# Kernel optimization log

Measured on AMD Instinct MI355X. Metric: run time of the kernel, lower is better.

The kernel has to match this reference:

```python
import jax, jax.numpy as jnp
import numpy as np
import math

D_MODEL = 1024
NUM_HEADS = 16
HEAD_DIM = D_MODEL // NUM_HEADS  # 64
THETA = 10000.0
BATCH = 2
SEQ = 2048


def setup_inputs() -> dict:
    key = jax.random.key(0)
    ks = jax.random.split(key, 5)
    scale = 0.02
    return {
        "in_features": jax.random.normal(ks[0], (BATCH, SEQ, D_MODEL), jnp.float32),
        "q_proj": jax.random.normal(ks[1], (D_MODEL, D_MODEL), jnp.float32) * scale,
        "k_proj": jax.random.normal(ks[2], (D_MODEL, D_MODEL), jnp.float32) * scale,
        "v_proj": jax.random.normal(ks[3], (D_MODEL, D_MODEL), jnp.float32) * scale,
        "o_proj": jax.random.normal(ks[4], (D_MODEL, D_MODEL), jnp.float32) * scale,
        "token_positions": jnp.arange(SEQ, dtype=jnp.int32),
    }


def _rope(x, token_positions):
    # x: [b, h, s, head_dim]; interleaved even/odd rotation
    half = HEAD_DIM // 2
    inv_freq = 1.0 / (THETA ** (2.0 * jnp.arange(half, dtype=x.dtype) / HEAD_DIM))
    angle = token_positions.astype(x.dtype)[:, None] * inv_freq[None, :]  # [s, half]
    cos, sin = jnp.cos(angle), jnp.sin(angle)
    x_e, x_o = x[..., ::2], x[..., 1::2]
    r_e = x_e * cos - x_o * sin
    r_o = x_e * sin + x_o * cos
    # interleave back: [..., s, half, 2] -> [..., s, head_dim]
    return jnp.stack([r_e, r_o], axis=-1).reshape(x.shape)


def reference(in_features, q_proj, k_proj, v_proj, o_proj, token_positions):
    b, s, _ = in_features.shape
    # projections: weight layout is [d_out, d_in]
    Q = jnp.einsum('bsd,kd->bsk', in_features, q_proj)
    K = jnp.einsum('bsd,kd->bsk', in_features, k_proj)
    V = jnp.einsum('bsd,kd->bsk', in_features, v_proj)
    # split heads: [b, h, s, head_dim]
    Q = Q.reshape(b, s, NUM_HEADS, HEAD_DIM).transpose(0, 2, 1, 3)
    K = K.reshape(b, s, NUM_HEADS, HEAD_DIM).transpose(0, 2, 1, 3)
    V = V.reshape(b, s, NUM_HEADS, HEAD_DIM).transpose(0, 2, 1, 3)
    Q = _rope(Q, token_positions)
    K = _rope(K, token_positions)
    scores = jnp.einsum('bhnd,bhmd->bhnm', Q, K) / math.sqrt(HEAD_DIM)
    causal = jnp.tril(jnp.ones((s, s), dtype=bool))  # [s, s]
    scores = jnp.where(causal[None, None], scores, -jnp.inf)
    attn = jax.nn.softmax(scores, axis=-1)
    out = jnp.einsum('bhnm,bhmd->bhnd', attn, V)
    out = out.transpose(0, 2, 1, 3).reshape(b, s, D_MODEL)
    return jnp.einsum('bsv,dv->bsd', out, o_proj)
```

## Files before the change

### kernel.cpp

```cpp
#include <hip/hip_runtime.h>
#include <hip/hip_bf16.h>

#define D_MODEL 1024
#define NHEAD   16
#define HDIM    64
#define SEQQ    2048
#define NBATCH  2
#define MROWS   (NBATCH * SEQQ)

typedef unsigned short u16;
typedef __attribute__((ext_vector_type(8))) short short8;
typedef __attribute__((ext_vector_type(4))) short short4v;
typedef __attribute__((ext_vector_type(4))) float floatx4;

__device__ __forceinline__ u16 f2b(float f) {
    union { __hip_bfloat16 h; u16 u; } cv;
    cv.h = __float2bfloat16(f);
    return cv.u;
}
__device__ __forceinline__ float b2f(u16 u) {
    return __uint_as_float(((unsigned int)u) << 16);
}
__device__ __forceinline__ short8 load8(const u16* p) {
    return *reinterpret_cast<const short8*>(p);
}
__device__ __forceinline__ short4v load4(const u16* p) {
    return *reinterpret_cast<const short4v*>(p);
}
__device__ __forceinline__ floatx4 mfma16(short4v a, short4v b, floatx4 c) {
#if __has_builtin(__builtin_amdgcn_mfma_f32_16x16x16bf16_1k)
    return __builtin_amdgcn_mfma_f32_16x16x16bf16_1k(a, b, c, 0, 0, 0);
#else
    floatx4 d;
    asm("v_mfma_f32_16x16x16_bf16 %0, %1, %2, %3"
        : "=v"(d) : "v"(a), "v"(b), "v"(c));
    return d;
#endif
}
__device__ __forceinline__ void async_cp16(const void* g, void* l) {
    __builtin_amdgcn_global_load_lds(
        (const __attribute__((address_space(1))) void*)g,
        (__attribute__((address_space(3))) void*)l, 16, 0, 0);
}

__global__ void cvt_all(const float* __restrict__ X,
                        const float* __restrict__ w0, const float* __restrict__ w1,
                        const float* __restrict__ w2, const float* __restrict__ w3,
                        u16* __restrict__ xo,
                        u16* __restrict__ o0, u16* __restrict__ o1,
                        u16* __restrict__ o2, u16* __restrict__ o3) {
    const int z = blockIdx.y;
    const int n4 = (D_MODEL * D_MODEL) / 4;
    const float* in;
    u16* out;
    if (z < 4) { in = X + (size_t)z * n4 * 4;  out = xo + (size_t)z * n4 * 4; }
    else {
        in  = (z == 4) ? w0 : (z == 5) ? w1 : (z == 6) ? w2 : w3;
        out = (z == 4) ? o0 : (z == 5) ? o1 : (z == 6) ? o2 : o3;
    }
    const int i = blockIdx.x * 256 + threadIdx.x;
    float4 v = reinterpret_cast<const float4*>(in)[i];
    ushort4 o;
    o.x = f2b(v.x); o.y = f2b(v.y); o.z = f2b(v.z); o.w = f2b(v.w);
    reinterpret_cast<ushort4*>(out)[i] = o;
}

__global__ __launch_bounds__(256) void gemm_qkv(
    const u16* __restrict__ A,
    const u16* __restrict__ B0, const u16* __restrict__ B1, const u16* __restrict__ B2,
    u16* __restrict__ C0, u16* __restrict__ C1, u16* __restrict__ C2)
{
    const int K = D_MODEL, N = D_MODEL;
    const u16* Bt = (blockIdx.z == 0) ? B0 : (blockIdx.z == 1 ? B1 : B2);
    u16*       Cp = (blockIdx.z == 0) ? C0 : (blockIdx.z == 1 ? C1 : C2);

    __shared__ __attribute__((aligned(16))) u16 As[128 * 32];
    __shared__ __attribute__((aligned(16))) u16 Bs[128 * 32];

    const int tid  = threadIdx.x;
    const int w    = tid >> 6;
    const int lane = tid & 63;
    const int l15  = lane & 15;
    const int quad = lane >> 4;
    const int wm   = w >> 1, wn = w & 1;
    const int tm   = blockIdx.x * 128, tn = blockIdx.y * 128;

    floatx4 acc[4][4];
#pragma unroll
    for (int i = 0; i < 4; i++)
#pragma unroll
        for (int j = 0; j < 4; j++) {
            floatx4 z = {0.f, 0.f, 0.f, 0.f};
            acc[i][j] = z;
        }

    const int srow = lane >> 2;
    const int scol = (lane & 3) * 8;

    for (int k0 = 0; k0 < K; k0 += 32) {
#pragma unroll
        for (int ch = w; ch < 8; ch += 4) {
            async_cp16(A  + (size_t)(tm + ch * 16 + srow) * K + k0 + scol, &As[ch * 512]);
            async_cp16(Bt + (size_t)(tn + ch * 16 + srow) * K + k0 + scol, &Bs[ch * 512]);
        }
        __syncthreads();

        short8 af[4], bfr[4];
#pragma unroll
        for (int mi = 0; mi < 4; mi++)
            af[mi] = load8(&As[(wm * 64 + mi * 16 + l15) * 32 + quad * 8]);
#pragma unroll
        for (int ni = 0; ni < 4; ni++)
            bfr[ni] = load8(&Bs[(wn * 64 + ni * 16 + l15) * 32 + quad * 8]);
#pragma unroll
        for (int mi = 0; mi < 4; mi++)
#pragma unroll
            for (int ni = 0; ni < 4; ni++)
                acc[mi][ni] = __builtin_amdgcn_mfma_f32_16x16x32_bf16(af[mi], bfr[ni], acc[mi][ni], 0, 0, 0);
        __syncthreads();
    }

#pragma unroll
    for (int mi = 0; mi < 4; mi++)
#pragma unroll
        for (int ni = 0; ni < 4; ni++)
#pragma unroll
            for (int rg = 0; rg < 4; rg++) {
                int row = tm + wm * 64 + mi * 16 + quad * 4 + rg;
                int col = tn + wn * 64 + ni * 16 + l15;
                Cp[(size_t)row * N + col] = f2b(acc[mi][ni][rg]);
            }
}

__global__ void rope_qk(const u16* __restrict__ Qraw, const u16* __restrict__ Kraw,
                        const int* __restrict__ pos, u16* __restrict__ Qt, u16* __restrict__ Kt)
{
    const int gid = blockIdx.x * 256 + threadIdx.x;
    const int j = gid & 31;
    const int s = (gid >> 5) & (SEQQ - 1);
    const int h = (gid >> 16) & (NHEAD - 1);
    const int b = gid >> 20;

    const float p   = (float)pos[s];
    const float inv = expf(-(float)j * (9.210340371976184f / 32.0f));
    float sn, cs;
    sincosf(p * inv, &sn, &cs);

    const size_t ioff = ((size_t)(b * SEQQ + s)) * D_MODEL + h * HDIM + 2 * j;
    const ushort2 qp = *reinterpret_cast<const ushort2*>(&Qraw[ioff]);
    const ushort2 kp = *reinterpret_cast<const ushort2*>(&Kraw[ioff]);
    const float qe = b2f(qp.x), qo = b2f(qp.y);
    const float ke = b2f(kp.x), ko = b2f(kp.y);

    const size_t ooff = (((size_t)(b * NHEAD + h)) * SEQQ + s) * HDIM + 2 * j;
    ushort2 qr;
    qr.x = f2b((qe * cs - qo * sn) * 0.125f);
    qr.y = f2b((qe * sn + qo * cs) * 0.125f);
    ushort2 kr;
    kr.x = f2b(ke * cs - ko * sn);
    kr.y = f2b(ke * sn + ko * cs);
    *reinterpret_cast<ushort2*>(&Qt[ooff]) = qr;
    *reinterpret_cast<ushort2*>(&Kt[ooff]) = kr;
}

__global__ __launch_bounds__(256) void vtrans(const u16* __restrict__ Vraw, u16* __restrict__ Vt)
{
    __shared__ u16 tile[64][65];
    const int s0 = blockIdx.x * 64, h = blockIdx.y, b = blockIdx.z;
    const int t = threadIdx.x;
#pragma unroll
    for (int i = 0; i < 16; i++) {
        int idx = t + i * 256;
        int sl = idx >> 6, dl = idx & 63;
        tile[sl][dl] = Vraw[((size_t)(b * SEQQ + s0 + sl)) * D_MODEL + h * HDIM + dl];
    }
    __syncthreads();
#pragma unroll
    for (int i = 0; i < 16; i++) {
        int idx = t + i * 256;
        int dl = idx >> 6, sl = idx & 63;
        Vt[(((size_t)(b * NHEAD + h)) * HDIM + dl) * SEQQ + s0 + sl] = tile[sl][dl];
    }
}

__global__ __launch_bounds__(256, 4) void attn_kernel(
    const u16* __restrict__ Qt, const u16* __restrict__ Kt, const u16* __restrict__ Vt,
    u16* __restrict__ Out)
{
    const int qblk = (gridDim.x - 1) - blockIdx.x;
    const int h = blockIdx.y, b = blockIdx.z;
    const int tid = threadIdx.x, w = tid >> 6, lane = tid & 63;
    const int l15 = lane & 15, quad = lane >> 4;
    const size_t bh = (size_t)(b * NHEAD + h);
    const u16* Qh = Qt + bh * SEQQ * HDIM;
    const u16* Kh = Kt + bh * SEQQ * HDIM;
    const u16* Vh = Vt + bh * HDIM * SEQQ;
    const int q0w = qblk * 64 + w * 16;

    __shared__ __attribute__((aligned(16))) u16 Ks[2][64 * 64];
    __shared__ __attribute__((aligned(16))) u16 Vs[2][64 * 64];

    short8 qf[2];
#pragma unroll
    for (int kk = 0; kk < 2; kk++)
        qf[kk] = load8(&Qh[(size_t)(q0w + l15) * HDIM + kk * 32 + quad * 8]);

    floatx4 Ot[4];
#pragma unroll
    for (int c = 0; c < 4; c++) { floatx4 z = {0.f, 0.f, 0.f, 0.f}; Ot[c] = z; }
    float lpart = 0.f;

    const int rr  = lane >> 3;
    const int swz = ((lane & 7) ^ rr) * 8;
    auto stage = [&](int buf, int tt) {
        const int k0s = tt * 64;
#pragma unroll
        for (int ch = w; ch < 8; ch += 4) {
            async_cp16(Kh + (size_t)(k0s + ch * 8 + rr) * HDIM + swz, &Ks[buf][ch * 512]);
            async_cp16(Vh + (size_t)(ch * 8 + rr) * SEQQ + k0s + swz, &Vs[buf][ch * 512]);
        }
    };

    const int sw1 = ((quad)     ^ (l15 & 7)) * 8;
    const int sw2 = ((quad + 4) ^ (l15 & 7)) * 8;

    stage(0, 0);

    for (int t = 0; t <= qblk; ++t) {
        __syncthreads();
        if (t < qblk) stage((t + 1) & 1, t + 1);

        const u16* KsB = &Ks[t & 1][0];
        const u16* VsB = &Vs[t & 1][0];
        const int k0 = t * 64;

        floatx4 St[4];
#pragma unroll
        for (int c = 0; c < 4; c++) {
            const int rowb = (c * 16 + l15) * 64;
            floatx4 z = {0.f, 0.f, 0.f, 0.f};
            St[c] = __builtin_amdgcn_mfma_f32_16x16x32_bf16(load8(&KsB[rowb + sw1]), qf[0], z,     0, 0, 0);
            St[c] = __builtin_amdgcn_mfma_f32_16x16x32_bf16(load8(&KsB[rowb + sw2]), qf[1], St[c], 0, 0, 0);
        }

        if (t == qblk) {
#pragma unroll
            for (int c = 0; c < 4; c++)
#pragma unroll
                for (int r = 0; r < 4; r++)
                    if (k0 + c * 16 + quad * 4 + r > q0w + l15) St[c][r] = -1e30f;
        }

        short4v pb[4];
#pragma unroll
        for (int c = 0; c < 4; c++) {
#pragma unroll
            for (int r = 0; r < 4; r++) {
                St[c][r] = __expf(St[c][r]);
                lpart += St[c][r];
            }
            short4v p;
            p[0] = (short)f2b(St[c][0]); p[1] = (short)f2b(St[c][1]);
            p[2] = (short)f2b(St[c][2]); p[3] = (short)f2b(St[c][3]);
            pb[c] = p;
        }

#pragma unroll
        for (int c2 = 0; c2 < 4; c2++) {
            const int base = (c2 * 16 + l15) * 64 + (quad & 1) * 4;
#pragma unroll
            for (int kw = 0; kw < 4; kw++) {
                const short4v va = load4(&VsB[base + ((kw * 2 + (quad >> 1)) ^ (l15 & 7)) * 8]);
                Ot[c2] = mfma16(va, pb[kw], Ot[c2]);
            }
        }
    }

    lpart += __shfl_xor(lpart, 16, 64);
    lpart += __shfl_xor(lpart, 32, 64);
    const float inv = 1.0f / lpart;

    const size_t orow = (size_t)(b * SEQQ + q0w + l15) * D_MODEL + h * HDIM;
#pragma unroll
    for (int c2 = 0; c2 < 4; c2++) {
        ushort4 o;
        o.x = f2b(Ot[c2][0] * inv); o.y = f2b(Ot[c2][1] * inv);
        o.z = f2b(Ot[c2][2] * inv); o.w = f2b(Ot[c2][3] * inv);
        *reinterpret_cast<ushort4*>(&Out[orow + c2 * 16 + quad * 4]) = o;
    }
}

__global__ __launch_bounds__(256) void gemm_o(
    const u16* __restrict__ A, const u16* __restrict__ Bt, float* __restrict__ C)
{
    const int K = D_MODEL, N = D_MODEL;
    __shared__ __attribute__((aligned(16))) u16 As[64 * 32];
    __shared__ __attribute__((aligned(16))) u16 Bs[128 * 32];

    const int tid  = threadIdx.x;
    const int w    = tid >> 6;
    const int lane = tid & 63;
    const int l15  = lane & 15;
    const int quad = lane >> 4;
    const int wm   = w >> 1, wn = w & 1;
    const int tm   = blockIdx.x * 64, tn = blockIdx.y * 128;

    floatx4 acc[2][4];
#pragma unroll
    for (int i = 0; i < 2; i++)
#pragma unroll
        for (int j = 0; j < 4; j++) {
            floatx4 z = {0.f, 0.f, 0.f, 0.f};
            acc[i][j] = z;
        }

    const int srow = lane >> 2;
    const int scol = (lane & 3) * 8;

    for (int k0 = 0; k0 < K; k0 += 32) {
#pragma unroll
        for (int ch = w; ch < 12; ch += 4) {
            if (ch < 4) async_cp16(A  + (size_t)(tm + ch * 16 + srow) * K + k0 + scol, &As[ch * 512]);
            else        async_cp16(Bt + (size_t)(tn + (ch - 4) * 16 + srow) * K + k0 + scol, &Bs[(ch - 4) * 512]);
        }
        __syncthreads();

        short8 af[2], bfr[4];
#pragma unroll
        for (int mi = 0; mi < 2; mi++)
            af[mi] = load8(&As[(wm * 32 + mi * 16 + l15) * 32 + quad * 8]);
#pragma unroll
        for (int ni = 0; ni < 4; ni++)
            bfr[ni] = load8(&Bs[(wn * 64 + ni * 16 + l15) * 32 + quad * 8]);
#pragma unroll
        for (int mi = 0; mi < 2; mi++)
#pragma unroll
            for (int ni = 0; ni < 4; ni++)
                acc[mi][ni] = __builtin_amdgcn_mfma_f32_16x16x32_bf16(af[mi], bfr[ni], acc[mi][ni], 0, 0, 0);
        __syncthreads();
    }

#pragma unroll
    for (int mi = 0; mi < 2; mi++)
#pragma unroll
        for (int ni = 0; ni < 4; ni++)
#pragma unroll
            for (int rg = 0; rg < 4; rg++) {
                int row = tm + wm * 32 + mi * 16 + quad * 4 + rg;
                int col = tn + wn * 64 + ni * 16 + l15;
                C[(size_t)row * N + col] = acc[mi][ni][rg];
            }
}

extern "C" void kernel_launch(void* const* d_in, const int* in_sizes, int n_in,
                              void* d_out, int out_size, void* d_ws, size_t ws_size,
                              hipStream_t stream)
{
    const float* X  = (const float*)d_in[0];
    const float* Wq = (const float*)d_in[1];
    const float* Wk = (const float*)d_in[2];
    const float* Wv = (const float*)d_in[3];
    const float* Wo = (const float*)d_in[4];
    const int* tpos = (const int*)d_in[5];
    float* out = (float*)d_out;
    char* ws = (char*)d_ws;

    const size_t MB = (size_t)1 << 20;
    u16* Xb   = (u16*)(ws + 0);
    u16* WqB  = (u16*)(ws + 8 * MB);
    u16* WkB  = (u16*)(ws + 10 * MB);
    u16* WvB  = (u16*)(ws + 12 * MB);
    u16* WoB  = (u16*)(ws + 14 * MB);
    u16* Qraw = (u16*)(ws + 16 * MB);
    u16* Kraw = (u16*)(ws + 24 * MB);
    u16* Vraw = (u16*)(ws + 32 * MB);
    u16* Qt   = (u16*)(ws + 40 * MB);
    u16* Kt   = (u16*)(ws + 48 * MB);
    u16* Vt   = Xb;
    u16* AOut = Qraw;

    cvt_all<<<dim3(1024, 8), 256, 0, stream>>>(X, Wq, Wk, Wv, Wo,
                                               Xb, WqB, WkB, WvB, WoB);

    gemm_qkv<<<dim3(32, 8, 3), 256, 0, stream>>>(Xb, WqB, WkB, WvB,
                                                 Qraw, Kraw, Vraw);
    rope_qk<<<8192, 256, 0, stream>>>(Qraw, Kraw, tpos, Qt, Kt);
    vtrans<<<dim3(32, 16, 2), 256, 0, stream>>>(Vraw, Vt);
    attn_kernel<<<dim3(32, 16, 2), 256, 0, stream>>>(Qt, Kt, Vt, AOut);
    gemm_o<<<dim3(64, 8), 256, 0, stream>>>(AOut, WoB, out);
}
```

Baseline: 205.4 us.

## Double attention query tile per block and widen QKV GEMM K-step with swizzled LDS

The attention kernel now gives each wave 32 query rows instead of 16, so each block covers 128 queries. Every K/V tile loaded into LDS is reused across twice as many MFMAs, and the grid is halved. Waves whose rows end before the current key tile skip compute, but they still take part in staging and barriers. The QKV GEMM moves to a 64-wide K step with an XOR-swizzled LDS layout, which halves the number of barriers and aims to reduce bank conflicts. In exchange, register pressure rises (occupancy hint lowered to 3) and the causal workload is less balanced across waves.

New measurement: 207.5 us. No clear change (+1.0%).

```diff
diff --git a/kernel.cpp b/kernel.cpp
--- a/kernel.cpp
+++ b/kernel.cpp
@@ -74,8 +74,8 @@
     const u16* Bt = (blockIdx.z == 0) ? B0 : (blockIdx.z == 1 ? B1 : B2);
     u16*       Cp = (blockIdx.z == 0) ? C0 : (blockIdx.z == 1 ? C1 : C2);
 
-    __shared__ __attribute__((aligned(16))) u16 As[128 * 32];
-    __shared__ __attribute__((aligned(16))) u16 Bs[128 * 32];
+    __shared__ __attribute__((aligned(16))) u16 As[128 * 64];
+    __shared__ __attribute__((aligned(16))) u16 Bs[128 * 64];
 
     const int tid  = threadIdx.x;
     const int w    = tid >> 6;
@@ -94,29 +94,33 @@
             acc[i][j] = z;
         }
 
-    const int srow = lane >> 2;
-    const int scol = (lane & 3) * 8;
-
-    for (int k0 = 0; k0 < K; k0 += 32) {
-#pragma unroll
-        for (int ch = w; ch < 8; ch += 4) {
-            async_cp16(A  + (size_t)(tm + ch * 16 + srow) * K + k0 + scol, &As[ch * 512]);
-            async_cp16(Bt + (size_t)(tn + ch * 16 + srow) * K + k0 + scol, &Bs[ch * 512]);
+    const int rr  = lane >> 3;
+    const int swz = ((lane & 7) ^ rr) * 8;
+
+    for (int k0 = 0; k0 < K; k0 += 64) {
+#pragma unroll
+        for (int ch = w; ch < 16; ch += 4) {
+            async_cp16(A  + (size_t)(tm + ch * 8 + rr) * K + k0 + swz, &As[ch * 512]);
+            async_cp16(Bt + (size_t)(tn + ch * 8 + rr) * K + k0 + swz, &Bs[ch * 512]);
         }
         __syncthreads();
 
-        short8 af[4], bfr[4];
-#pragma unroll
-        for (int mi = 0; mi < 4; mi++)
-            af[mi] = load8(&As[(wm * 64 + mi * 16 + l15) * 32 + quad * 8]);
-#pragma unroll
-        for (int ni = 0; ni < 4; ni++)
-            bfr[ni] = load8(&Bs[(wn * 64 + ni * 16 + l15) * 32 + quad * 8]);
-#pragma unroll
-        for (int mi = 0; mi < 4; mi++)
+#pragma unroll
+        for (int kk = 0; kk < 2; kk++) {
+            const int rsw = ((quad + 4 * kk) ^ (l15 & 7)) * 8;
+            short8 af[4], bfr[4];
+#pragma unroll
+            for (int mi = 0; mi < 4; mi++)
+                af[mi] = load8(&As[(wm * 64 + mi * 16 + l15) * 64 + rsw]);
 #pragma unroll
             for (int ni = 0; ni < 4; ni++)
-                acc[mi][ni] = __builtin_amdgcn_mfma_f32_16x16x32_bf16(af[mi], bfr[ni], acc[mi][ni], 0, 0, 0);
+                bfr[ni] = load8(&Bs[(wn * 64 + ni * 16 + l15) * 64 + rsw]);
+#pragma unroll
+            for (int mi = 0; mi < 4; mi++)
+#pragma unroll
+                for (int ni = 0; ni < 4; ni++)
+                    acc[mi][ni] = __builtin_amdgcn_mfma_f32_16x16x32_bf16(af[mi], bfr[ni], acc[mi][ni], 0, 0, 0);
+        }
         __syncthreads();
     }
 
@@ -183,7 +187,7 @@
     }
 }
 
-__global__ __launch_bounds__(256, 4) void attn_kernel(
+__global__ __launch_bounds__(256, 3) void attn_kernel(
     const u16* __restrict__ Qt, const u16* __restrict__ Kt, const u16* __restrict__ Vt,
     u16* __restrict__ Out)
 {
@@ -195,20 +199,27 @@
     const u16* Qh = Qt + bh * SEQQ * HDIM;
     const u16* Kh = Kt + bh * SEQQ * HDIM;
     const u16* Vh = Vt + bh * HDIM * SEQQ;
-    const int q0w = qblk * 64 + w * 16;
+    const int q0w = qblk * 128 + w * 32;
+    const int tdiag = q0w >> 6;
+    const int tmax  = qblk * 2 + 1;
 
     __shared__ __attribute__((aligned(16))) u16 Ks[2][64 * 64];
     __shared__ __attribute__((aligned(16))) u16 Vs[2][64 * 64];
 
-    short8 qf[2];
-#pragma unroll
-    for (int kk = 0; kk < 2; kk++)
-        qf[kk] = load8(&Qh[(size_t)(q0w + l15) * HDIM + kk * 32 + quad * 8]);
-
-    floatx4 Ot[4];
-#pragma unroll
-    for (int c = 0; c < 4; c++) { floatx4 z = {0.f, 0.f, 0.f, 0.f}; Ot[c] = z; }
-    float lpart = 0.f;
+    short8 qfA[2], qfB[2];
+#pragma unroll
+    for (int kk = 0; kk < 2; kk++) {
+        qfA[kk] = load8(&Qh[(size_t)(q0w + l15) * HDIM + kk * 32 + quad * 8]);
+        qfB[kk] = load8(&Qh[(size_t)(q0w + 16 + l15) * HDIM + kk * 32 + quad * 8]);
+    }
+
+    floatx4 OtA[4], OtB[4];
+#pragma unroll
+    for (int c = 0; c < 4; c++) {
+        floatx4 z = {0.f, 0.f, 0.f, 0.f};
+        OtA[c] = z; OtB[c] = z;
+    }
+    float lA = 0.f, lB = 0.f;
 
     const int rr  = lane >> 3;
     const int swz = ((lane & 7) ^ rr) * 8;
@@ -226,43 +237,54 @@
 
     stage(0, 0);
 
-    for (int t = 0; t <= qblk; ++t) {
+    for (int t = 0; t <= tmax; ++t) {
         __syncthreads();
-        if (t < qblk) stage((t + 1) & 1, t + 1);
+        if (t < tmax) stage((t + 1) & 1, t + 1);
+
+        if (t > tdiag) continue;
 
         const u16* KsB = &Ks[t & 1][0];
         const u16* VsB = &Vs[t & 1][0];
         const int k0 = t * 64;
 
-        floatx4 St[4];
+        floatx4 SA[4], SB[4];
 #pragma unroll
         for (int c = 0; c < 4; c++) {
             const int rowb = (c * 16 + l15) * 64;
+            const short8 ka = load8(&KsB[rowb + sw1]);
+            const short8 kb = load8(&KsB[rowb + sw2]);
             floatx4 z = {0.f, 0.f, 0.f, 0.f};
-            St[c] = __builtin_amdgcn_mfma_f32_16x16x32_bf16(load8(&KsB[rowb + sw1]), qf[0], z,     0, 0, 0);
-            St[c] = __builtin_amdgcn_mfma_f32_16x16x32_bf16(load8(&KsB[rowb + sw2]), qf[1], St[c], 0, 0, 0);
-        }
-
-        if (t == qblk) {
+            SA[c] = __builtin_amdgcn_mfma_f32_16x16x32_bf16(ka, qfA[0], z,     0, 0, 0);
+            SA[c] = __builtin_amdgcn_mfma_f32_16x16x32_bf16(kb, qfA[1], SA[c], 0, 0, 0);
+            SB[c] = __builtin_amdgcn_mfma_f32_16x16x32_bf16(ka, qfB[0], z,     0, 0, 0);
+            SB[c] = __builtin_amdgcn_mfma_f32_16x16x32_bf16(kb, qfB[1], SB[c], 0, 0, 0);
+        }
+
+        if (t == tdiag) {
 #pragma unroll
             for (int c = 0; c < 4; c++)
 #pragma unroll
-                for (int r = 0; r < 4; r++)
-                    if (k0 + c * 16 + quad * 4 + r > q0w + l15) St[c][r] = -1e30f;
-        }
-
-        short4v pb[4];
+                for (int r = 0; r < 4; r++) {
+                    const int key = k0 + c * 16 + quad * 4 + r;
+                    if (key > q0w + l15)      SA[c][r] = -1e30f;
+                    if (key > q0w + 16 + l15) SB[c][r] = -1e30f;
+                }
+        }
+
+        short4v pbA[4], pbB[4];
 #pragma unroll
         for (int c = 0; c < 4; c++) {
 #pragma unroll
             for (int r = 0; r < 4; r++) {
-                St[c][r] = __expf(St[c][r]);
-                lpart += St[c][r];
+                SA[c][r] = __expf(SA[c][r]);  lA += SA[c][r];
+                SB[c][r] = __expf(SB[c][r]);  lB += SB[c][r];
             }
-            short4v p;
-            p[0] = (short)f2b(St[c][0]); p[1] = (short)f2b(St[c][1]);
-            p[2] = (short)f2b(St[c][2]); p[3] = (short)f2b(St[c][3]);
-            pb[c] = p;
+            short4v pa, pb;
+            pa[0] = (short)f2b(SA[c][0]); pa[1] = (short)f2b(SA[c][1]);
+            pa[2] = (short)f2b(SA[c][2]); pa[3] = (short)f2b(SA[c][3]);
+            pb[0] = (short)f2b(SB[c][0]); pb[1] = (short)f2b(SB[c][1]);
+            pb[2] = (short)f2b(SB[c][2]); pb[3] = (short)f2b(SB[c][3]);
+            pbA[c] = pa; pbB[c] = pb;
         }
 
 #pragma unroll
@@ -271,22 +293,30 @@
 #pragma unroll
             for (int kw = 0; kw < 4; kw++) {
                 const short4v va = load4(&VsB[base + ((kw * 2 + (quad >> 1)) ^ (l15 & 7)) * 8]);
-                Ot[c2] = mfma16(va, pb[kw], Ot[c2]);
+                OtA[c2] = mfma16(va, pbA[kw], OtA[c2]);
+                OtB[c2] = mfma16(va, pbB[kw], OtB[c2]);
             }
         }
     }
 
-    lpart += __shfl_xor(lpart, 16, 64);
-    lpart += __shfl_xor(lpart, 32, 64);
-    const float inv = 1.0f / lpart;
-
-    const size_t orow = (size_t)(b * SEQQ + q0w + l15) * D_MODEL + h * HDIM;
+    lA += __shfl_xor(lA, 16, 64);
+    lA += __shfl_xor(lA, 32, 64);
+    lB += __shfl_xor(lB, 16, 64);
+    lB += __shfl_xor(lB, 32, 64);
+    const float invA = 1.0f / lA;
+    const float invB = 1.0f / lB;
+
+    const size_t orowA = (size_t)(b * SEQQ + q0w + l15) * D_MODEL + h * HDIM;
+    const size_t orowB = (size_t)(b * SEQQ + q0w + 16 + l15) * D_MODEL + h * HDIM;
 #pragma unroll
     for (int c2 = 0; c2 < 4; c2++) {
-        ushort4 o;
-        o.x = f2b(Ot[c2][0] * inv); o.y = f2b(Ot[c2][1] * inv);
-        o.z = f2b(Ot[c2][2] * inv); o.w = f2b(Ot[c2][3] * inv);
-        *reinterpret_cast<ushort4*>(&Out[orow + c2 * 16 + quad * 4]) = o;
+        ushort4 oa, ob;
+        oa.x = f2b(OtA[c2][0] * invA); oa.y = f2b(OtA[c2][1] * invA);
+        oa.z = f2b(OtA[c2][2] * invA); oa.w = f2b(OtA[c2][3] * invA);
+        ob.x = f2b(OtB[c2][0] * invB); ob.y = f2b(OtB[c2][1] * invB);
+        ob.z = f2b(OtB[c2][2] * invB); ob.w = f2b(OtB[c2][3] * invB);
+        *reinterpret_cast<ushort4*>(&Out[orowA + c2 * 16 + quad * 4]) = oa;
+        *reinterpret_cast<ushort4*>(&Out[orowB + c2 * 16 + quad * 4]) = ob;
     }
 }
 
@@ -386,6 +416,6 @@
                                                  Qraw, Kraw, Vraw);
     rope_qk<<<8192, 256, 0, stream>>>(Qraw, Kraw, tpos, Qt, Kt);
     vtrans<<<dim3(32, 16, 2), 256, 0, stream>>>(Vraw, Vt);
-    attn_kernel<<<dim3(32, 16, 2), 256, 0, stream>>>(Qt, Kt, Vt, AOut);
+    attn_kernel<<<dim3(16, 16, 2), 256, 0, stream>>>(Qt, Kt, Vt, AOut);
     gemm_o<<<dim3(64, 8), 256, 0, stream>>>(AOut, WoB, out);
 }
```
